# Performance work log

Hardware: AMD Instinct MI355X
Metric: run time of the kernel (lower is better)

Reference implementation:

```python
import jax, jax.numpy as jnp
from jax import lax
import numpy as np

B, N, NPOINT, NSAMPLE = 16, 4096, 1024, 32
RADIUS = 0.2
D_FEAT = 64
IN_CH = 3 + D_FEAT
MLP = (64, 64, 128)
EPS = 1e-5


def fps(xyz, npoint):
    # farthest point sampling, xyz: [B,N,3] -> idx [B,npoint] (start at index 0)
    Bn, Nn, _ = xyz.shape
    batch = jnp.arange(Bn)

    def step(carry, _):
        dist, far = carry                      # dist [B,N], far [B]
        centroid = xyz[batch, far]             # [B,3]
        d = jnp.sum((xyz - centroid[:, None, :]) ** 2, -1)
        dist = jnp.minimum(dist, d)
        new_far = jnp.argmax(dist, -1).astype(jnp.int32)
        return (dist, new_far), far

    init = (jnp.full((Bn, Nn), 1e10, xyz.dtype), jnp.zeros((Bn,), jnp.int32))
    _, idxs = lax.scan(step, init, None, length=npoint)
    return jnp.transpose(idxs)                 # [B, npoint]


def square_distance(a, b):
    # a [B,S,3], b [B,N,3] -> [B,S,N]
    return (jnp.sum(a * a, -1)[:, :, None]
            + jnp.sum(b * b, -1)[:, None, :]
            - 2.0 * jnp.einsum('bsc,bnc->bsn', a, b))


def query_ball(radius, nsample, xyz, new_xyz):
    Nn = xyz.shape[1]
    sqr = square_distance(new_xyz, xyz)                      # [B,S,N]
    gi = jnp.where(sqr > radius ** 2, Nn, jnp.arange(Nn, dtype=jnp.int32))
    gi = jnp.sort(gi, axis=-1)[:, :, :nsample]               # [B,S,K]
    first = gi[:, :, :1]
    return jnp.where(gi == Nn, first, gi)


def gather_points(pts, idx):
    # pts [B,N,C], idx [B,...] -> [B,...,C]
    return jax.vmap(lambda p, i: p[i])(pts, idx)


def _forward(xyz, points, params):
    x = jnp.transpose(xyz, (0, 2, 1))          # [B,N,3]
    p = jnp.transpose(points, (0, 2, 1))       # [B,N,D]
    fidx = fps(x, NPOINT)                      # [B,S]
    new_xyz = gather_points(x, fidx)           # [B,S,3]
    idx = query_ball(RADIUS, NSAMPLE, x, new_xyz)  # [B,S,K]
    g_xyz = gather_points(x, idx)              # [B,S,K,3]
    g_norm = g_xyz - new_xyz[:, :, None, :]
    g_pts = gather_points(p, idx)              # [B,S,K,D]
    feat = jnp.concatenate([g_norm, g_pts], -1)  # [B,S,K,3+D]
    h = jnp.transpose(feat, (0, 3, 2, 1))      # [B,C,K,S]
    for (w, b, g, bt) in params:
        h = jnp.einsum('bcks,oc->boks', h, w) + b[None, :, None, None]
        m = jnp.mean(h, axis=(0, 2, 3), keepdims=True)
        v = jnp.mean((h - m) ** 2, axis=(0, 2, 3), keepdims=True)  # biased var (train BN)
        h = g[None, :, None, None] * (h - m) * lax.rsqrt(v + EPS) + bt[None, :, None, None]
        h = jax.nn.relu(h)
    new_points = jnp.max(h, axis=2)            # [B,Cout,S]
    return jnp.transpose(new_xyz, (0, 2, 1)), new_points


def setup_inputs() -> dict:
    key = jax.random.key(0)
    ks = jax.random.split(key, 16)
    xyz = jax.random.uniform(ks[0], (B, 3, N), dtype=jnp.float32)
    points = jax.random.normal(ks[1], (B, D_FEAT, N), dtype=jnp.float32)
    inp = {'xyz': xyz, 'points': points}
    cin = IN_CH
    for l, cout in enumerate(MLP):
        scale = 1.0 / np.sqrt(cin)
        inp[f'w{l}'] = jax.random.normal(ks[2 + 4 * l], (cout, cin), dtype=jnp.float32) * scale
        inp[f'b{l}'] = jax.random.normal(ks[3 + 4 * l], (cout,), dtype=jnp.float32) * scale
        inp[f'g{l}'] = jnp.ones((cout,), jnp.float32)
        inp[f'bt{l}'] = jnp.zeros((cout,), jnp.float32)
        cin = cout
    return inp


def reference(xyz, points, w0, b0, g0, bt0, w1, b1, g1, bt1, w2, b2, g2, bt2):
    params = [(w0, b0, g0, bt0), (w1, b1, g1, bt1), (w2, b2, g2, bt2)]
    return _forward(xyz, points, params)
```

## Files before the change

### kernel.cpp

```cpp
#include <hip/hip_runtime.h>
#include <stdint.h>

#define NB    16
#define NN    4096
#define NP    1024
#define NS    32
#define NGRP  (NB*NP)
#define CNT   524288.0

typedef short  bf16x8 __attribute__((ext_vector_type(8)));
typedef float  f32x4  __attribute__((ext_vector_type(4)));
typedef float  f32x2  __attribute__((ext_vector_type(2)));

__device__ __forceinline__ float bf2f(unsigned short u) {
    return __uint_as_float(((unsigned)u) << 16);
}
__device__ __forceinline__ unsigned short f2bf(float f) {
    unsigned u = __float_as_uint(f);
    unsigned r = u + 0x7fffu + ((u >> 16) & 1u);
    return (unsigned short)(r >> 16);
}
__device__ __forceinline__ bf16x8 as_bf(uint4 u) {
    union { uint4 a; bf16x8 b; } c; c.a = u; return c.b;
}

template <int CTRL, int RM>
__device__ __forceinline__ unsigned long long dppmax(unsigned long long k) {
    int lo = (int)(unsigned)k;
    int hi = (int)(k >> 32);
    int ml = __builtin_amdgcn_update_dpp(lo, lo, CTRL, RM, 0xf, false);
    int mh = __builtin_amdgcn_update_dpp(hi, hi, CTRL, RM, 0xf, false);
    unsigned long long m = ((unsigned long long)(unsigned)mh << 32) | (unsigned)ml;
    return m > k ? m : k;
}

__global__ __launch_bounds__(256, 1) void fps_t_kernel(const float* __restrict__ xyz,
                                                       const float* __restrict__ points,
                                                       const float* __restrict__ w0,
                                                       int* __restrict__ fidx,
                                                       unsigned short* __restrict__ T) {
    if (blockIdx.x >= 16) {
        int gid = (blockIdx.x - 16) * 256 + threadIdx.x;
        int b = gid >> 12, n = gid & (NN - 1);
        const float* xb = xyz + (size_t)b * 3 * NN;
        const float* pb = points + (size_t)b * 64 * NN;
        float acc[64];
#pragma unroll
        for (int o = 0; o < 64; o++) acc[o] = 0.f;
        for (int c = 0; c < 67; c++) {
            float v = (c < 3) ? xb[c * NN + n] : pb[(c - 3) * NN + n];
#pragma unroll
            for (int o = 0; o < 64; o++) acc[o] = fmaf(v, w0[o * 67 + c], acc[o]);
        }
        unsigned short* dst = T + (size_t)gid * 64;
        for (int oo = 0; oo < 64; oo += 8) {
            union { unsigned short u[8]; uint4 v; } r;
#pragma unroll
            for (int j = 0; j < 8; j++) r.u[j] = f2bf(acc[oo + j]);
            *(uint4*)&dst[oo] = r.v;
        }
        return;
    }
    int b = blockIdx.x, tid = threadIdx.x;
    const float* xb = xyz + (size_t)b * 3 * NN;
    __shared__ float4 sxyz4[NN];
    __shared__ unsigned long long red[2][4];
    __shared__ int fbuf[NP];
    f32x2 px2[8], py2[8], pz2[8], dist2[8];
#pragma unroll
    for (int i = 0; i < 16; i++) {
        int n = i * 256 + tid;
        float x = xb[n], y = xb[NN + n], z = xb[2 * NN + n];
        px2[i >> 1][i & 1] = x;
        py2[i >> 1][i & 1] = y;
        pz2[i >> 1][i & 1] = z;
        sxyz4[n] = make_float4(x, y, z, 0.f);
        dist2[i >> 1][i & 1] = 1e10f;
    }
#pragma unroll
    for (int i = 0; i < 8; i++) {
        asm volatile("" : "+v"(px2[i]));
        asm volatile("" : "+v"(py2[i]));
        asm volatile("" : "+v"(pz2[i]));
    }
    int wv = tid >> 6;
    if (tid == 0) fbuf[0] = 0;
    int far = 0;
    __syncthreads();
    for (int t = 0; t < NP; t++) {
        float4 c = sxyz4[far];
        f32x2 cx2 = {c.x, c.x};
        f32x2 cy2 = {c.y, c.y};
        f32x2 cz2 = {c.z, c.z};
        float bv = -1.0f; int bi = 0;
        {
#pragma clang fp contract(off)
#pragma unroll
            for (int i2 = 0; i2 < 8; i2++) {
                f32x2 dx = px2[i2] - cx2;
                f32x2 dy = py2[i2] - cy2;
                f32x2 dz = pz2[i2] - cz2;
                f32x2 xx = dx * dx;
                f32x2 yy = dy * dy;
                f32x2 zz = dz * dz;
                f32x2 d  = (xx + yy) + zz;
                float nd0 = fminf(dist2[i2][0], d[0]);
                float nd1 = fminf(dist2[i2][1], d[1]);
                dist2[i2][0] = nd0;
                dist2[i2][1] = nd1;
                if (nd0 > bv) { bv = nd0; bi = 2 * i2; }
                if (nd1 > bv) { bv = nd1; bi = 2 * i2 + 1; }
            }
        }
        int n_best = bi * 256 + tid;
        unsigned long long k =
            ((unsigned long long)__float_as_uint(bv) << 32) |
            (unsigned long long)(~(unsigned)n_best);
        k = dppmax<0x111, 0xf>(k);
        k = dppmax<0x112, 0xf>(k);
        k = dppmax<0x114, 0xf>(k);
        k = dppmax<0x118, 0xf>(k);
        k = dppmax<0x142, 0xa>(k);
        k = dppmax<0x143, 0xc>(k);
        if ((tid & 63) == 63) red[t & 1][wv] = k;
        __syncthreads();
        ulonglong2 ra = *(ulonglong2*)&red[t & 1][0];
        ulonglong2 rb = *(ulonglong2*)&red[t & 1][2];
        unsigned long long r0 = ra.x, r1 = ra.y, r2 = rb.x, r3 = rb.y;
        if (r1 > r0) r0 = r1;
        if (r3 > r2) r2 = r3;
        if (r2 > r0) r0 = r2;
        far = (int)(~(unsigned)r0);
        if (tid == 0 && t + 1 < NP) fbuf[t + 1] = far;
    }
    __syncthreads();
    for (int i = tid; i < NP; i += 256) fidx[b * NP + i] = fbuf[i];
}

__global__ __launch_bounds__(256) void group_kernel(const float* __restrict__ xyz,
                                                    const unsigned short* __restrict__ T,
                                                    const int* __restrict__ fidx,
                                                    int* __restrict__ idx,
                                                    const float* __restrict__ w0,
                                                    const float* __restrict__ b0,
                                                    double* __restrict__ stage1,
                                                    float* __restrict__ out0) {
    __shared__ int gidx[4][NS];
    int t = threadIdx.x, wv = t >> 6, lane = t & 63;
    int g = blockIdx.x * 4 + wv;
    int b = g >> 10, s = g & 1023;
    const float* xb = xyz + (size_t)b * 3 * NN;
    int fid = fidx[g];
    float cx = xb[fid], cy = xb[NN + fid], cz = xb[2 * NN + fid];
    if (lane < 3) {
        float v = (lane == 0) ? cx : ((lane == 1) ? cy : cz);
        out0[((size_t)b * 3 + lane) * NP + s] = v;
    }
    float sa = __fadd_rn(__fadd_rn(__fmul_rn(cx, cx), __fmul_rn(cy, cy)),
                         __fmul_rn(cz, cz));
    int* out = idx + (size_t)g * NS;
    int total = 0; int first = 0;
    for (int ci = 0; ci < NN / 64; ci++) {
        int n = ci * 64 + lane;
        float x = xb[n], y = xb[NN + n], z = xb[2 * NN + n];
        float sb = __fadd_rn(__fadd_rn(__fmul_rn(x, x), __fmul_rn(y, y)),
                             __fmul_rn(z, z));
        float dot = __fadd_rn(__fadd_rn(__fmul_rn(x, cx), __fmul_rn(y, cy)),
                              __fmul_rn(z, cz));
        float sqr = __fsub_rn(__fadd_rn(sa, sb), __fmul_rn(2.0f, dot));
        bool pred = !(sqr > 0.04f);
        unsigned long long mask = __ballot(pred);
        if (mask) {
            if (total == 0) first = ci * 64 + (int)__builtin_ctzll(mask);
            int pos = total + (int)__popcll(mask & ((1ull << lane) - 1ull));
            if (pred && pos < NS) { out[pos] = n; gidx[wv][pos] = n; }
            total += (int)__popcll(mask);
            if (total >= NS) break;
        }
    }
    if (total < NS) {
        if (lane >= total && lane < NS) { out[lane] = first; gidx[wv][lane] = first; }
    }
    int o = lane;
    float uo = fmaf(w0[o * 67 + 2], cz, fmaf(w0[o * 67 + 1], cy, w0[o * 67] * cx));
    float bo = b0[o];
    const unsigned short* Tb = T + (size_t)b * NN * 64;
    float s1 = 0.f, s2 = 0.f;
    for (int k = 0; k < NS; k++) {
        int n = gidx[wv][k];
        float tv = bf2f(Tb[(size_t)n * 64 + o]);
        float h = tv - uo + bo;
        s1 += h; s2 = fmaf(h, h, s2);
    }
    int slot = g & 63;
    atomicAdd(&stage1[slot * 128 + o], (double)s1);
    atomicAdd(&stage1[slot * 128 + 64 + o], (double)s2);
}

__global__ void finalize_kernel(const double* __restrict__ stage, int C,
                                const float* __restrict__ gamma,
                                const float* __restrict__ beta,
                                float* __restrict__ AB) {
    int o = threadIdx.x;
    double s = 0.0, q = 0.0;
    for (int i = 0; i < 64; i++) {
        s += stage[i * 2 * C + o];
        q += stage[i * 2 * C + C + o];
    }
    double m = s * (1.0 / CNT);
    double v = q * (1.0 / CNT) - m * m;
    double A = (double)gamma[o] / sqrt(v + 1e-5);
    AB[o] = (float)A;
    AB[C + o] = (float)((double)beta[o] - m * A);
}

__global__ __launch_bounds__(256) void layer2_kernel(const float* __restrict__ xyz,
                                                     const unsigned short* __restrict__ T,
                                                     const int* __restrict__ fidx,
                                                     const int* __restrict__ idx,
                                                     const float* __restrict__ w0,
                                                     const float* __restrict__ b0,
                                                     const float* __restrict__ AB1,
                                                     const float* __restrict__ w1,
                                                     const float* __restrict__ b1,
                                                     unsigned short* __restrict__ h2,
                                                     double* __restrict__ stage2) {
    __shared__ __attribute__((aligned(16))) unsigned short w1s[64][72];
    __shared__ __attribute__((aligned(16))) unsigned short h1s[4][32][72];
    __shared__ float psum[64], psq[64];
    int t = threadIdx.x, wv = t >> 6, lane = t & 63;
    int quad = lane >> 4, col = lane & 15;
    int g = blockIdx.x * 4 + wv;
    int b = g >> 10;
    for (int lin = t; lin < 4096; lin += 256)
        w1s[lin >> 6][lin & 63] = f2bf(w1[lin]);
    if (t < 64) { psum[t] = 0.f; psq[t] = 0.f; }
    {
        int fid = fidx[g];
        const float* xb = xyz + (size_t)b * 3 * NN;
        float cx = xb[fid], cy = xb[NN + fid], cz = xb[2 * NN + fid];
        int o = lane;
        float uo = fmaf(w0[o * 67 + 2], cz, fmaf(w0[o * 67 + 1], cy, w0[o * 67] * cx));
        float bo = b0[o];
        float a1 = AB1[o], bb1 = AB1[64 + o];
        const int* gi = idx + (size_t)g * NS;
        const unsigned short* Tb = T + (size_t)b * NN * 64;
        for (int k = 0; k < NS; k++) {
            int n = gi[k];
            float tv = bf2f(Tb[(size_t)n * 64 + o]);
            float h = tv - uo + bo;
            float hn = fmaxf(fmaf(h, a1, bb1), 0.f);
            h1s[wv][k][o] = f2bf(hn);
        }
    }
    __syncthreads();
    f32x4 acc[2][4];
#pragma unroll
    for (int i = 0; i < 2; i++)
#pragma unroll
        for (int j = 0; j < 4; j++) acc[i][j] = (f32x4){0.f, 0.f, 0.f, 0.f};
#pragma unroll
    for (int ks = 0; ks < 2; ks++) {
        bf16x8 a0 = as_bf(*(const uint4*)&h1s[wv][col][ks * 32 + quad * 8]);
        bf16x8 a1f = as_bf(*(const uint4*)&h1s[wv][16 + col][ks * 32 + quad * 8]);
#pragma unroll
        for (int nt = 0; nt < 4; nt++) {
            bf16x8 bf = as_bf(*(const uint4*)&w1s[nt * 16 + col][ks * 32 + quad * 8]);
            acc[0][nt] = __builtin_amdgcn_mfma_f32_16x16x32_bf16(a0, bf, acc[0][nt], 0, 0, 0);
            acc[1][nt] = __builtin_amdgcn_mfma_f32_16x16x32_bf16(a1f, bf, acc[1][nt], 0, 0, 0);
        }
    }
    float s1[4], s2[4];
#pragma unroll
    for (int nt = 0; nt < 4; nt++) {
        float bb = b1[nt * 16 + col];
        s1[nt] = 0.f; s2[nt] = 0.f;
#pragma unroll
        for (int mt = 0; mt < 2; mt++)
#pragma unroll
            for (int r = 0; r < 4; r++) {
                float v = acc[mt][nt][r] + bb;
                s1[nt] += v; s2[nt] = fmaf(v, v, s2[nt]);
                h1s[wv][mt * 16 + quad * 4 + r][nt * 16 + col] = f2bf(v);
            }
        s1[nt] += __shfl_xor(s1[nt], 16); s1[nt] += __shfl_xor(s1[nt], 32);
        s2[nt] += __shfl_xor(s2[nt], 16); s2[nt] += __shfl_xor(s2[nt], 32);
        if (quad == 0) {
            atomicAdd(&psum[nt * 16 + col], s1[nt]);
            atomicAdd(&psq[nt * 16 + col], s2[nt]);
        }
    }
#pragma unroll
    for (int r = 0; r < 4; r++) {
        int lin = lane + 64 * r;
        int row = lin >> 3, c = lin & 7;
        uint4 v = *(const uint4*)&h1s[wv][row][c * 8];
        *(uint4*)&h2[((size_t)g * NS + row) * 64 + c * 8] = v;
    }
    __syncthreads();
    if (t < 64) {
        int slot = blockIdx.x & 63;
        atomicAdd(&stage2[slot * 128 + t], (double)psum[t]);
        atomicAdd(&stage2[slot * 128 + 64 + t], (double)psq[t]);
    }
}

__global__ __launch_bounds__(256) void layer3_kernel(const unsigned short* __restrict__ h2,
                                                     const float* __restrict__ AB2,
                                                     const float* __restrict__ w2,
                                                     const float* __restrict__ b2,
                                                     double* __restrict__ stage3,
                                                     float* __restrict__ mxbuf,
                                                     float* __restrict__ mnbuf) {
    __shared__ __attribute__((aligned(16))) unsigned short w2s[128][72];
    __shared__ __attribute__((aligned(16))) unsigned short h2s[4][32][72];
    __shared__ float psum[128], psq[128];
    int t = threadIdx.x, wv = t >> 6, lane = t & 63;
    int quad = lane >> 4, col = lane & 15;
    int g = blockIdx.x * 4 + wv;
    for (int lin = t; lin < 8192; lin += 256)
        w2s[lin >> 6][lin & 63] = f2bf(w2[lin]);
    if (t < 128) { psum[t] = 0.f; psq[t] = 0.f; }
    {
        int c = lane & 7;
        float a2v[8], bb2v[8];
#pragma unroll
        for (int j = 0; j < 8; j++) {
            a2v[j] = AB2[c * 8 + j];
            bb2v[j] = AB2[64 + c * 8 + j];
        }
        const unsigned short* hg = h2 + (size_t)g * NS * 64;
#pragma unroll
        for (int r = 0; r < 4; r++) {
            int row = (lane >> 3) + 8 * r;
            union { uint4 v; unsigned short u[8]; } in, outp;
            in.v = *(const uint4*)&hg[row * 64 + c * 8];
#pragma unroll
            for (int j = 0; j < 8; j++) {
                float f = bf2f(in.u[j]);
                outp.u[j] = f2bf(fmaxf(fmaf(f, a2v[j], bb2v[j]), 0.f));
            }
            *(uint4*)&h2s[wv][row][c * 8] = outp.v;
        }
    }
    __syncthreads();
    f32x4 acc[2][8];
#pragma unroll
    for (int i = 0; i < 2; i++)
#pragma unroll
        for (int j = 0; j < 8; j++) acc[i][j] = (f32x4){0.f, 0.f, 0.f, 0.f};
#pragma unroll
    for (int ks = 0; ks < 2; ks++) {
        bf16x8 a0 = as_bf(*(const uint4*)&h2s[wv][col][ks * 32 + quad * 8]);
        bf16x8 a1f = as_bf(*(const uint4*)&h2s[wv][16 + col][ks * 32 + quad * 8]);
#pragma unroll
        for (int nt = 0; nt < 8; nt++) {
            bf16x8 bf = as_bf(*(const uint4*)&w2s[nt * 16 + col][ks * 32 + quad * 8]);
            acc[0][nt] = __builtin_amdgcn_mfma_f32_16x16x32_bf16(a0, bf, acc[0][nt], 0, 0, 0);
            acc[1][nt] = __builtin_amdgcn_mfma_f32_16x16x32_bf16(a1f, bf, acc[1][nt], 0, 0, 0);
        }
    }
#pragma unroll
    for (int nt = 0; nt < 8; nt++) {
        float bb = b2[nt * 16 + col];
        float s1 = 0.f, s2 = 0.f, mx = -1e30f, mn = 1e30f;
#pragma unroll
        for (int mt = 0; mt < 2; mt++)
#pragma unroll
            for (int r = 0; r < 4; r++) {
                float v = acc[mt][nt][r] + bb;
                s1 += v; s2 = fmaf(v, v, s2);
                mx = fmaxf(mx, v); mn = fminf(mn, v);
            }
        s1 += __shfl_xor(s1, 16); s1 += __shfl_xor(s1, 32);
        s2 += __shfl_xor(s2, 16); s2 += __shfl_xor(s2, 32);
        mx = fmaxf(mx, __shfl_xor(mx, 16)); mx = fmaxf(mx, __shfl_xor(mx, 32));
        mn = fminf(mn, __shfl_xor(mn, 16)); mn = fminf(mn, __shfl_xor(mn, 32));
        if (quad == 0) {
            atomicAdd(&psum[nt * 16 + col], s1);
            atomicAdd(&psq[nt * 16 + col], s2);
            mxbuf[(size_t)g * 128 + nt * 16 + col] = mx;
            mnbuf[(size_t)g * 128 + nt * 16 + col] = mn;
        }
    }
    __syncthreads();
    if (t < 128) {
        int slot = blockIdx.x & 63;
        atomicAdd(&stage3[slot * 256 + t], (double)psum[t]);
        atomicAdd(&stage3[slot * 256 + 128 + t], (double)psq[t]);
    }
}

__global__ __launch_bounds__(256) void epilogue_kernel(const float* __restrict__ mxbuf,
                                                       const float* __restrict__ mnbuf,
                                                       const float* __restrict__ AB3,
                                                       float* __restrict__ out1) {
    __shared__ float tile[32][65];
    int blk = blockIdx.x;
    int b = blk >> 6; int rem = blk & 63;
    int o0 = (rem >> 4) * 32; int s0 = (rem & 15) * 64;
    int t = threadIdx.x;
#pragma unroll
    for (int j = 0; j < 8; j++) {
        int lin = t + 256 * j;
        int sl = lin >> 5, ol = lin & 31;
        int o = o0 + ol;
        float a = AB3[o], bb = AB3[128 + o];
        size_t src = ((size_t)b * NP + s0 + sl) * 128 + o;
        float v = (a >= 0.f) ? mxbuf[src] : mnbuf[src];
        tile[ol][sl] = fmaxf(fmaf(v, a, bb), 0.f);
    }
    __syncthreads();
#pragma unroll
    for (int j = 0; j < 8; j++) {
        int lin = t + 256 * j;
        int ol = lin >> 6, sl = lin & 63;
        out1[((size_t)b * 128 + o0 + ol) * NP + s0 + sl] = tile[ol][sl];
    }
}

extern "C" void kernel_launch(void* const* d_in, const int* in_sizes, int n_in,
                              void* d_out, int out_size, void* d_ws, size_t ws_size,
                              hipStream_t stream) {
    const float* xyz    = (const float*)d_in[0];
    const float* points = (const float*)d_in[1];
    const float* w0  = (const float*)d_in[2];
    const float* b0  = (const float*)d_in[3];
    const float* g0  = (const float*)d_in[4];
    const float* bt0 = (const float*)d_in[5];
    const float* w1  = (const float*)d_in[6];
    const float* b1  = (const float*)d_in[7];
    const float* g1  = (const float*)d_in[8];
    const float* bt1 = (const float*)d_in[9];
    const float* w2  = (const float*)d_in[10];
    const float* b2  = (const float*)d_in[11];
    const float* g2  = (const float*)d_in[12];
    const float* bt2 = (const float*)d_in[13];

    char* ws = (char*)d_ws;
    int*            fidx = (int*)(ws + 0);
    int*            idx  = (int*)(ws + 65536);
    unsigned short* T    = (unsigned short*)(ws + 2162688);
    unsigned short* h2   = (unsigned short*)(ws + 10551296);
    float*          mxbuf = (float*)(ws + 77660160);
    float*          mnbuf = (float*)(ws + 86048768);
    double*         stage = (double*)(ws + 94437376);
    float*          AB   = (float*)(ws + 94699520);
    double* stage1 = stage;
    double* stage2 = stage + 64 * 128;
    double* stage3 = stage + 2 * 64 * 128;
    float* AB1 = AB; float* AB2 = AB + 128; float* AB3 = AB + 256;
    float* out0 = (float*)d_out;
    float* out1 = out0 + NB * 3 * NP;

    hipMemsetAsync(stage, 0, 262144, stream);

    fps_t_kernel<<<16 + 256, 256, 0, stream>>>(xyz, points, w0, fidx, T);
    group_kernel<<<NGRP / 4, 256, 0, stream>>>(xyz, T, fidx, idx, w0, b0, stage1, out0);
    finalize_kernel<<<1, 64, 0, stream>>>(stage1, 64, g0, bt0, AB1);
    layer2_kernel<<<NGRP / 4, 256, 0, stream>>>(xyz, T, fidx, idx, w0, b0, AB1,
                                                w1, b1, h2, stage2);
    finalize_kernel<<<1, 64, 0, stream>>>(stage2, 64, g1, bt1, AB2);
    layer3_kernel<<<NGRP / 4, 256, 0, stream>>>(h2, AB2, w2, b2, stage3, mxbuf, mnbuf);
    finalize_kernel<<<1, 128, 0, stream>>>(stage3, 128, g2, bt2, AB3);
    epilogue_kernel<<<1024, 256, 0, stream>>>(mxbuf, mnbuf, AB3, out1);
}
```

Before: 848.2 us.

## Carry winning point coordinates through FPS reduction instead of shared-memory lookup

The farthest-point-sampling loop no longer stages all xyz in shared memory and reads the next centroid by index after the reduction. Each lane now carries the coordinates of its best candidate through a select-based tree, and the winning lane of each wave writes its key plus xyz to shared memory. The final cross-wave max then yields the next centroid directly, which removes the dependent LDS load on the serial critical path and the 64KB shared array. The cost is extra select instructions, more registers per lane, and a readlane comparison to find the winning lane.

```diff
diff --git a/kernel.cpp b/kernel.cpp
--- a/kernel.cpp
+++ b/kernel.cpp
@@ -63,19 +63,19 @@
     }
     int b = blockIdx.x, tid = threadIdx.x;
     const float* xb = xyz + (size_t)b * 3 * NN;
-    __shared__ float4 sxyz4[NN];
-    __shared__ unsigned long long red[2][4];
+    __shared__ __attribute__((aligned(16))) unsigned int red32[2][4][8];
     __shared__ int fbuf[NP];
     f32x2 px2[8], py2[8], pz2[8], dist2[8];
+    unsigned int klo[16];
+    unsigned int ntid = ~(unsigned)tid;
 #pragma unroll
     for (int i = 0; i < 16; i++) {
         int n = i * 256 + tid;
-        float x = xb[n], y = xb[NN + n], z = xb[2 * NN + n];
-        px2[i >> 1][i & 1] = x;
-        py2[i >> 1][i & 1] = y;
-        pz2[i >> 1][i & 1] = z;
-        sxyz4[n] = make_float4(x, y, z, 0.f);
+        px2[i >> 1][i & 1] = xb[n];
+        py2[i >> 1][i & 1] = xb[NN + n];
+        pz2[i >> 1][i & 1] = xb[2 * NN + n];
         dist2[i >> 1][i & 1] = 1e10f;
+        klo[i] = ntid - (unsigned)(i * 256);
     }
 #pragma unroll
     for (int i = 0; i < 8; i++) {
@@ -85,14 +85,12 @@
     }
     int wv = tid >> 6;
     if (tid == 0) fbuf[0] = 0;
-    int far = 0;
-    __syncthreads();
+    float cx = xb[0], cy = xb[NN], cz = xb[2 * NN];
     for (int t = 0; t < NP; t++) {
-        float4 c = sxyz4[far];
-        f32x2 cx2 = {c.x, c.x};
-        f32x2 cy2 = {c.y, c.y};
-        f32x2 cz2 = {c.z, c.z};
-        float bv = -1.0f; int bi = 0;
+        f32x2 cx2 = {cx, cx};
+        f32x2 cy2 = {cy, cy};
+        f32x2 cz2 = {cz, cz};
+        float nd[16];
         {
 #pragma clang fp contract(off)
 #pragma unroll
@@ -104,34 +102,92 @@
                 f32x2 yy = dy * dy;
                 f32x2 zz = dz * dz;
                 f32x2 d  = (xx + yy) + zz;
-                float nd0 = fminf(dist2[i2][0], d[0]);
-                float nd1 = fminf(dist2[i2][1], d[1]);
-                dist2[i2][0] = nd0;
-                dist2[i2][1] = nd1;
-                if (nd0 > bv) { bv = nd0; bi = 2 * i2; }
-                if (nd1 > bv) { bv = nd1; bi = 2 * i2 + 1; }
+                float n0 = fminf(dist2[i2][0], d[0]);
+                float n1 = fminf(dist2[i2][1], d[1]);
+                dist2[i2][0] = n0;
+                dist2[i2][1] = n1;
+                nd[2 * i2] = n0;
+                nd[2 * i2 + 1] = n1;
             }
         }
-        int n_best = bi * 256 + tid;
-        unsigned long long k =
-            ((unsigned long long)__float_as_uint(bv) << 32) |
-            (unsigned long long)(~(unsigned)n_best);
+        unsigned long long K8[8]; float X8[8], Y8[8], Z8[8];
+#pragma unroll
+        for (int i = 0; i < 8; i++) {
+            unsigned long long ka = ((unsigned long long)__float_as_uint(nd[2 * i]) << 32)
+                                  | (unsigned long long)klo[2 * i];
+            unsigned long long kb = ((unsigned long long)__float_as_uint(nd[2 * i + 1]) << 32)
+                                  | (unsigned long long)klo[2 * i + 1];
+            bool w = kb > ka;
+            K8[i] = w ? kb : ka;
+            X8[i] = w ? px2[i][1] : px2[i][0];
+            Y8[i] = w ? py2[i][1] : py2[i][0];
+            Z8[i] = w ? pz2[i][1] : pz2[i][0];
+        }
+        unsigned long long K4[4]; float X4[4], Y4[4], Z4[4];
+#pragma unroll
+        for (int i = 0; i < 4; i++) {
+            bool w = K8[2 * i + 1] > K8[2 * i];
+            K4[i] = w ? K8[2 * i + 1] : K8[2 * i];
+            X4[i] = w ? X8[2 * i + 1] : X8[2 * i];
+            Y4[i] = w ? Y8[2 * i + 1] : Y8[2 * i];
+            Z4[i] = w ? Z8[2 * i + 1] : Z8[2 * i];
+        }
+        unsigned long long K2[2]; float X2[2], Y2[2], Z2[2];
+#pragma unroll
+        for (int i = 0; i < 2; i++) {
+            bool w = K4[2 * i + 1] > K4[2 * i];
+            K2[i] = w ? K4[2 * i + 1] : K4[2 * i];
+            X2[i] = w ? X4[2 * i + 1] : X4[2 * i];
+            Y2[i] = w ? Y4[2 * i + 1] : Y4[2 * i];
+            Z2[i] = w ? Z4[2 * i + 1] : Z4[2 * i];
+        }
+        bool wf0 = K2[1] > K2[0];
+        unsigned long long myk = wf0 ? K2[1] : K2[0];
+        float bx = wf0 ? X2[1] : X2[0];
+        float by = wf0 ? Y2[1] : Y2[0];
+        float bz = wf0 ? Z2[1] : Z2[0];
+        unsigned long long k = myk;
         k = dppmax<0x111, 0xf>(k);
         k = dppmax<0x112, 0xf>(k);
         k = dppmax<0x114, 0xf>(k);
         k = dppmax<0x118, 0xf>(k);
         k = dppmax<0x142, 0xa>(k);
         k = dppmax<0x143, 0xc>(k);
-        if ((tid & 63) == 63) red[t & 1][wv] = k;
+        unsigned wlo = (unsigned)__builtin_amdgcn_readlane((int)(unsigned)k, 63);
+        unsigned whi = (unsigned)__builtin_amdgcn_readlane((int)(k >> 32), 63);
+        int p = t & 1;
+        if ((unsigned)myk == wlo && (unsigned)(myk >> 32) == whi) {
+            uint4 w4;
+            w4.x = (unsigned)myk;
+            w4.y = (unsigned)(myk >> 32);
+            w4.z = __float_as_uint(bx);
+            w4.w = __float_as_uint(by);
+            *(uint4*)&red32[p][wv][0] = w4;
+            red32[p][wv][4] = __float_as_uint(bz);
+        }
         __syncthreads();
-        ulonglong2 ra = *(ulonglong2*)&red[t & 1][0];
-        ulonglong2 rb = *(ulonglong2*)&red[t & 1][2];
-        unsigned long long r0 = ra.x, r1 = ra.y, r2 = rb.x, r3 = rb.y;
-        if (r1 > r0) r0 = r1;
-        if (r3 > r2) r2 = r3;
-        if (r2 > r0) r0 = r2;
-        far = (int)(~(unsigned)r0);
-        if (tid == 0 && t + 1 < NP) fbuf[t + 1] = far;
+        uint4 s0 = *(const uint4*)&red32[p][0][0];
+        uint4 s1 = *(const uint4*)&red32[p][1][0];
+        uint4 s2 = *(const uint4*)&red32[p][2][0];
+        uint4 s3 = *(const uint4*)&red32[p][3][0];
+        unsigned z0 = red32[p][0][4], z1 = red32[p][1][4];
+        unsigned z2 = red32[p][2][4], z3 = red32[p][3][4];
+        unsigned long long mk0 = ((unsigned long long)s0.y << 32) | s0.x;
+        unsigned long long mk1 = ((unsigned long long)s1.y << 32) | s1.x;
+        unsigned long long mk2 = ((unsigned long long)s2.y << 32) | s2.x;
+        unsigned long long mk3 = ((unsigned long long)s3.y << 32) | s3.x;
+        bool wA = mk1 > mk0;
+        unsigned long long kA = wA ? mk1 : mk0;
+        unsigned xA = wA ? s1.z : s0.z, yA = wA ? s1.w : s0.w, zA = wA ? z1 : z0;
+        bool wB = mk3 > mk2;
+        unsigned long long kB = wB ? mk3 : mk2;
+        unsigned xB = wB ? s3.z : s2.z, yB = wB ? s3.w : s2.w, zB = wB ? z3 : z2;
+        bool wF = kB > kA;
+        unsigned long long kF = wF ? kB : kA;
+        cx = __uint_as_float(wF ? xB : xA);
+        cy = __uint_as_float(wF ? yB : yA);
+        cz = __uint_as_float(wF ? zB : zA);
+        if (tid == 0 && t + 1 < NP) fbuf[t + 1] = (int)(~(unsigned)kF);
     }
     __syncthreads();
     for (int i = tid; i < NP; i += 256) fidx[b * NP + i] = fbuf[i];
```

Result: slower. 1.084 ms (+27.8%).
